# Performance work log

Hardware: AMD Instinct MI355X
Metric: run time of the kernel (lower is better)

The kernel has to match this reference:

```python
import jax, jax.numpy as jnp
import numpy as np

DIM = 384
HEADS = 12
HD = DIM // HEADS  # 32
WIN = 16
N = WIN * WIN      # 256
B = 256            # num_windows * batch
K = 5              # dwc kernel size
EPS = 1e-6


def setup_inputs() -> dict:
    key = jax.random.key(0)
    ks = jax.random.split(key, 8)
    u = lambda k, shape, fan_in: jax.random.uniform(
        k, shape, jnp.float32, -1.0 / np.sqrt(fan_in), 1.0 / np.sqrt(fan_in))
    return {
        "x": jax.random.normal(ks[0], (B, N, DIM), jnp.float32),
        # nn.Linear(dim, 3*dim): weight [3C, C], bias [3C]
        "qkv_w": u(ks[1], (3 * DIM, DIM), DIM),
        "qkv_b": u(ks[2], (3 * DIM,), DIM),
        # nn.Parameter initialized to zeros
        "pos_enc": jnp.zeros((1, N, DIM), jnp.float32),
        # depthwise Conv2d(HD, HD, K, groups=HD): weight [HD, 1, K, K]
        "dwc_w": u(ks[3], (HD, 1, K, K), K * K),
        "dwc_b": u(ks[4], (HD,), K * K),
        "proj_w": u(ks[5], (DIM, DIM), DIM),
        "proj_b": u(ks[6], (DIM,), DIM),
    }


def reference(x, qkv_w, qkv_b, pos_enc, dwc_w, dwc_b, proj_w, proj_b):
    Bsz, Nn, C = x.shape
    qkv = x @ qkv_w.T + qkv_b                     # [B, N, 3C]
    q, k, v = jnp.split(qkv, 3, axis=-1)          # each [B, N, C]
    k = k + pos_enc
    q = jax.nn.relu(q)
    k = jax.nn.relu(k)

    def to_heads(t):  # 'b n (h c) -> (b h) n c'
        return t.reshape(Bsz, Nn, HEADS, HD).transpose(0, 2, 1, 3).reshape(Bsz * HEADS, Nn, HD)

    q, k, v = to_heads(q), to_heads(k), to_heads(v)
    # explicit fp32 (autocast disabled block in original)
    qf = q.astype(jnp.float32)
    kf = k.astype(jnp.float32)
    vf = v.astype(jnp.float32)

    z = 1.0 / (jnp.einsum('bic,bc->bi', qf, kf.sum(axis=1)) + EPS)  # [BH, N]

    i = j = Nn
    c = d = HD
    if i * j * (c + d) > c * d * (i + j):  # kv-first (true for N=256, HD=32)
        kv = jnp.einsum('bjc,bjd->bcd', kf, vf)            # [BH, c, d]
        out = jnp.einsum('bic,bcd,bi->bid', qf, kv, z)     # [BH, N, d]
    else:
        qk = jnp.einsum('bic,bjc->bij', qf, kf)
        out = jnp.einsum('bij,bjd,bi->bid', qk, vf, z)

    # depthwise conv on v: 'b (w h) c -> b c w h'
    num = int(Nn ** 0.5)
    fm = vf.reshape(Bsz * HEADS, num, num, HD).transpose(0, 3, 1, 2)  # NCHW
    fm = jax.lax.conv_general_dilated(
        fm, dwc_w, window_strides=(1, 1),
        padding=[(K // 2, K // 2), (K // 2, K // 2)],
        dimension_numbers=('NCHW', 'OIHW', 'NCHW'),
        feature_group_count=HD)
    fm = fm + dwc_b[None, :, None, None]
    fm = fm.transpose(0, 2, 3, 1).reshape(Bsz * HEADS, Nn, HD)  # 'b c w h -> b (w h) c'

    out = out + fm
    # '(b h) n c -> b n (h c)'
    out = out.reshape(Bsz, HEADS, Nn, HD).transpose(0, 2, 1, 3).reshape(Bsz, Nn, C)
    return out @ proj_w.T + proj_b
```

## Files before the change

### kernel.cpp

```cpp
#include <hip/hip_runtime.h>
#include <stdint.h>
#include <stddef.h>


typedef _Float16 f16;
typedef __attribute__((ext_vector_type(4))) _Float16 f16x4;
typedef __attribute__((ext_vector_type(8))) _Float16 f16x8;
typedef __attribute__((ext_vector_type(4))) float floatx4;

#define DEV __device__ __forceinline__

DEV void async16(const void* g, void* l) {
  __builtin_amdgcn_global_load_lds(
      (const __attribute__((address_space(1))) void*)g,
      (__attribute__((address_space(3))) void*)l,
      16, 0, 0);
}

DEV floatx4 mfma16(f16x8 a, f16x8 b, floatx4 c) {
  return __builtin_amdgcn_mfma_f32_16x16x32_f16(a, b, c, 0, 0, 0);
}

DEV f16x4 cvt4(float4 v) {
  f16x4 h;
  h[0] = (f16)v.x; h[1] = (f16)v.y; h[2] = (f16)v.z; h[3] = (f16)v.w;
  return h;
}

__global__ __launch_bounds__(256) void cvt_kernel(
    const float* __restrict__ src, f16* __restrict__ dst, int n4) {
  const int stride = gridDim.x * 256;
  for (int i = blockIdx.x * 256 + threadIdx.x; i < n4; i += stride) {
    float4 v = ((const float4*)src)[i];
    ((f16x4*)dst)[i] = cvt4(v);
  }
}

__global__ __launch_bounds__(256) void qkv_kernel(
    const f16* __restrict__ A, const f16* __restrict__ W,
    const float* __restrict__ bias, const float* __restrict__ pos,
    f16* __restrict__ q_ws, f16* __restrict__ kT_ws, f16* __restrict__ vT_ws) {
  __shared__ __align__(16) f16 Af[128 * 64];
  __shared__ __align__(16) f16 Wf[128 * 64];
  const int tid = threadIdx.x;
  const int lane = tid & 63, wave = tid >> 6;
  const int quad = lane >> 4, lr = lane & 15;
  const int wm = wave >> 1, wn = wave & 1;
  const int bx = blockIdx.x;
  const int ga = bx / 72, rem = bx - ga * 72;
  const int nblk = rem >> 3, gc = rem & 7;
  const int m0 = (ga * 8 + gc) * 128, n0 = nblk * 128;
  const int rl = lane >> 3;
  const int lcol = (lane & 7) ^ rl;

  floatx4 acc[4][4] = {};

  const f16* ap[4];
  const f16* wp[4];
#pragma unroll
  for (int t2 = 0; t2 < 4; ++t2) {
    const int row = (wave * 4 + t2) * 8 + rl;
    ap[t2] = A + (size_t)(m0 + row) * 384 + lcol * 8;
    wp[t2] = W + (size_t)(n0 + row) * 384 + lcol * 8;
  }

  for (int kt = 0; kt < 6; ++kt) {
    __syncthreads();
#pragma unroll
    for (int t2 = 0; t2 < 4; ++t2) {
      const int ch = wave * 4 + t2;
      async16(ap[t2] + kt * 64, (char*)Af + ch * 1024);
      async16(wp[t2] + kt * 64, (char*)Wf + ch * 1024);
    }
    __syncthreads();
#pragma unroll
    for (int s = 0; s < 2; ++s) {
      const int pc = ((quad + s * 4) ^ (lr & 7)) * 16;
      f16x8 af[4], wf[4];
#pragma unroll
      for (int mt = 0; mt < 4; ++mt)
        af[mt] = *(const f16x8*)((const char*)Af +
                                 (wm * 64 + mt * 16 + lr) * 128 + pc);
#pragma unroll
      for (int nt = 0; nt < 4; ++nt)
        wf[nt] = *(const f16x8*)((const char*)Wf +
                                 (wn * 64 + nt * 16 + lr) * 128 + pc);
#pragma unroll
      for (int mt = 0; mt < 4; ++mt)
#pragma unroll
        for (int nt = 0; nt < 4; ++nt)
          acc[mt][nt] = mfma16(af[mt], wf[nt], acc[mt][nt]);
    }
  }

  float bv[4];
#pragma unroll
  for (int nt = 0; nt < 4; ++nt)
    bv[nt] = bias[n0 + wn * 64 + nt * 16 + lr];

  const int cls = nblk / 3;
  const int cbase = (nblk - cls * 3) * 128;
  if (cls == 0) {
#pragma unroll
    for (int mt = 0; mt < 4; ++mt) {
#pragma unroll
      for (int r = 0; r < 4; ++r) {
        const int m = m0 + wm * 64 + mt * 16 + quad * 4 + r;
        const int bwin = m >> 8, t = m & 255;
#pragma unroll
        for (int nt = 0; nt < 4; ++nt) {
          const int c = cbase + wn * 64 + nt * 16 + lr;
          const int h = c >> 5, hd = c & 31;
          const float val = fmaxf(acc[mt][nt][r] + bv[nt], 0.f);
          q_ws[(size_t)(bwin * 12 + h) * 8192 + t * 32 + hd] = (f16)val;
        }
      }
    }
  } else {
#pragma unroll
    for (int mt = 0; mt < 4; ++mt) {
      const int mb = m0 + wm * 64 + mt * 16 + quad * 4;
      const int bwin = mb >> 8, t0 = mb & 255;
#pragma unroll
      for (int nt = 0; nt < 4; ++nt) {
        const int c = cbase + wn * 64 + nt * 16 + lr;
        const int h = c >> 5, hd = c & 31;
        f16x4 pk;
        if (cls == 1) {
#pragma unroll
          for (int r = 0; r < 4; ++r)
            pk[r] = (f16)fmaxf(acc[mt][nt][r] + bv[nt] + pos[(t0 + r) * 384 + c], 0.f);
          *(f16x4*)(kT_ws + (size_t)(bwin * 12 + h) * 8192 + hd * 256 + t0) = pk;
        } else {
#pragma unroll
          for (int r = 0; r < 4; ++r)
            pk[r] = (f16)(acc[mt][nt][r] + bv[nt]);
          *(f16x4*)(vT_ws + (size_t)(bwin * 12 + h) * 8192 + hd * 256 + t0) = pk;
        }
      }
    }
  }
}

__global__ __launch_bounds__(256) void attn_kernel(
    const f16* __restrict__ q_ws, const f16* __restrict__ kT_ws,
    const f16* __restrict__ vT_ws, const float* __restrict__ dwc_w,
    const float* __restrict__ dwc_b, f16* __restrict__ y_ws) {
  __shared__ __align__(16) char khb[16640];
  __shared__ __align__(16) char vhb[16640];
  __shared__ float psum[8 * 32];
  __shared__ float ksum[4][32];
  __shared__ float zbuf[256];
  __shared__ __align__(16) f16 kvT[32 * 40];

  const int tid = threadIdx.x;
  const int lane = tid & 63, wave = tid >> 6;
  const int quad = lane >> 4, lr = lane & 15;
  const size_t base = (size_t)blockIdx.x * 8192;

#pragma unroll
  for (int t2 = 0; t2 < 4; ++t2) {
    const int is = wave * 4 + t2;
    async16(kT_ws + base + is * 512 + lane * 8, khb + is * 1040);
    async16(vT_ws + base + is * 512 + lane * 8, vhb + is * 1040);
  }
  __syncthreads();

  {
    const int c = tid & 31, seg = tid >> 5;
    const char* kr = khb + (c >> 1) * 1040 + (c & 1) * 512;
    float s = 0.f;
#pragma unroll
    for (int j8 = 0; j8 < 32; j8 += 8) {
      f16x8 a = *(const f16x8*)(kr + (seg * 32 + j8) * 2);
#pragma unroll
      for (int j = 0; j < 8; ++j) s += (float)a[j];
    }
    psum[seg * 32 + c] = s;
  }
  {
    const int m2 = wave & 1, n2 = wave >> 1;
    const int ck = m2 * 16 + lr, cv = n2 * 16 + lr;
    const char* krow = khb + (ck >> 1) * 1040 + (ck & 1) * 512;
    const char* vrow = vhb + (cv >> 1) * 1040 + (cv & 1) * 512;
    floatx4 kacc = {};
#pragma unroll
    for (int s = 0; s < 8; ++s) {
      f16x8 ka = *(const f16x8*)(krow + (s * 32 + quad * 8) * 2);
      f16x8 vb = *(const f16x8*)(vrow + (s * 32 + quad * 8) * 2);
      kacc = mfma16(ka, vb, kacc);
    }
    f16x4 kk;
#pragma unroll
    for (int r = 0; r < 4; ++r) kk[r] = (f16)kacc[r];
    *(f16x4*)(kvT + (n2 * 16 + lr) * 40 + m2 * 16 + quad * 4) = kk;
  }
  __syncthreads();

  if (lane < 32) {
    float s = 0.f;
#pragma unroll
    for (int seg = 0; seg < 8; ++seg) s += psum[seg * 32 + lane];
    ksum[wave][lane] = s;
  }

  {
    uint32_t* fmu = (uint32_t*)khb;
    const int cg = lr, xr = wave * 4 + quad, c0 = cg * 2;
    float a0[16], a1[16];
    const float b0v = dwc_b[c0], b1v = dwc_b[c0 + 1];
#pragma unroll
    for (int yy = 0; yy < 16; ++yy) { a0[yy] = b0v; a1[yy] = b1v; }
    const char* v0 = vhb + cg * 1040;
#pragma unroll
    for (int dx = 0; dx < 5; ++dx) {
      const int xx = xr + dx - 2;
      if (xx < 0 || xx > 15) continue;
      float r0[16], r1[16];
      f16x8 h0 = *(const f16x8*)(v0 + xx * 32);
      f16x8 h1 = *(const f16x8*)(v0 + xx * 32 + 16);
      f16x8 h2 = *(const f16x8*)(v0 + 512 + xx * 32);
      f16x8 h3 = *(const f16x8*)(v0 + 512 + xx * 32 + 16);
#pragma unroll
      for (int j = 0; j < 8; ++j) {
        r0[j] = (float)h0[j]; r0[8 + j] = (float)h1[j];
        r1[j] = (float)h2[j]; r1[8 + j] = (float)h3[j];
      }
#pragma unroll
      for (int dy = 0; dy < 5; ++dy) {
        const float w0 = dwc_w[c0 * 25 + dx * 5 + dy];
        const float w1 = dwc_w[(c0 + 1) * 25 + dx * 5 + dy];
#pragma unroll
        for (int yy = 0; yy < 16; ++yy) {
          const int ys = yy + dy - 2;
          if (ys >= 0 && ys < 16) {
            a0[yy] += w0 * r0[ys];
            a1[yy] += w1 * r1[ys];
          }
        }
      }
    }
#pragma unroll
    for (int yy = 0; yy < 16; ++yy) {
      const uint32_t lo = (uint32_t)__builtin_bit_cast(uint16_t, (f16)a0[yy]);
      const uint32_t hi = (uint32_t)__builtin_bit_cast(uint16_t, (f16)a1[yy]);
      fmu[(xr * 16 + yy) * 16 + cg] = lo | (hi << 16);
    }
  }

  {
    f16x8 qa[4], kb[2];
#pragma unroll
    for (int mm = 0; mm < 4; ++mm)
      qa[mm] = *(const f16x8*)(q_ws + base +
                               (size_t)(wave * 64 + mm * 16 + lr) * 32 + quad * 8);

    float ksv[8];
#pragma unroll
    for (int j = 0; j < 8; ++j) ksv[j] = ksum[wave][quad * 8 + j];
#pragma unroll
    for (int mm = 0; mm < 4; ++mm) {
      float dot = 0.f;
#pragma unroll
      for (int j = 0; j < 8; ++j) dot += (float)qa[mm][j] * ksv[j];
      dot += __shfl_xor(dot, 16);
      dot += __shfl_xor(dot, 32);
      if (quad == 0) zbuf[wave * 64 + mm * 16 + lr] = 1.f / (dot + 1e-6f);
    }

    floatx4 oacc[4][2] = {};
#pragma unroll
    for (int nt = 0; nt < 2; ++nt)
      kb[nt] = *(const f16x8*)(kvT + (nt * 16 + lr) * 40 + quad * 8);
#pragma unroll
    for (int mm = 0; mm < 4; ++mm)
#pragma unroll
      for (int nt = 0; nt < 2; ++nt)
        oacc[mm][nt] = mfma16(qa[mm], kb[nt], oacc[mm][nt]);

    const f16* fmb = (const f16*)khb;
#pragma unroll
    for (int mm = 0; mm < 4; ++mm) {
#pragma unroll
      for (int r = 0; r < 4; ++r) {
        const int i = wave * 64 + mm * 16 + quad * 4 + r;
        const float zi = zbuf[i];
#pragma unroll
        for (int nt = 0; nt < 2; ++nt) {
          const int d = nt * 16 + lr;
          const float val = oacc[mm][nt][r] * zi + (float)fmb[i * 32 + d];
          y_ws[base + (size_t)i * 32 + d] = (f16)val;
        }
      }
    }
  }
}

__global__ __launch_bounds__(256) void proj_kernel(
    const f16* __restrict__ Y, const f16* __restrict__ Wh,
    const float* __restrict__ bias, float* __restrict__ out) {
  __shared__ __align__(16) f16 Af[128 * 64];
  __shared__ __align__(16) f16 Wf[128 * 64];
  const int tid = threadIdx.x;
  const int lane = tid & 63, wave = tid >> 6;
  const int quad = lane >> 4, lr = lane & 15;
  const int wm = wave >> 1, wn = wave & 1;
  const int bx = blockIdx.x;
  const int ga = bx / 24, rem = bx - ga * 24;
  const int nblk = rem >> 3, gc = rem & 7;
  const int m0 = (ga * 8 + gc) * 128, n0 = nblk * 128;
  const int bwin = m0 >> 8, tbase = m0 & 255;
  const int rl = lane >> 3;
  const int lcol = (lane & 7) ^ rl;

  floatx4 acc[4][4] = {};

  const f16* ap[4];
  const f16* wp[4];
#pragma unroll
  for (int t2 = 0; t2 < 4; ++t2) {
    const int rowl = (wave * 4 + t2) * 8 + rl;
    ap[t2] = Y + (size_t)(bwin * 12 + (lcol >> 2)) * 8192 +
             (size_t)(tbase + rowl) * 32 + (lcol & 3) * 8;
    wp[t2] = Wh + (size_t)(n0 + rowl) * 384 + lcol * 8;
  }

  for (int kt = 0; kt < 6; ++kt) {
    __syncthreads();
#pragma unroll
    for (int t2 = 0; t2 < 4; ++t2) {
      const int ch = wave * 4 + t2;
      async16(ap[t2] + (size_t)kt * 16384, (char*)Af + ch * 1024);
      async16(wp[t2] + kt * 64, (char*)Wf + ch * 1024);
    }
    __syncthreads();
#pragma unroll
    for (int s = 0; s < 2; ++s) {
      const int pc = ((quad + s * 4) ^ (lr & 7)) * 16;
      f16x8 af[4], wf[4];
#pragma unroll
      for (int mt = 0; mt < 4; ++mt)
        af[mt] = *(const f16x8*)((const char*)Af +
                                 (wm * 64 + mt * 16 + lr) * 128 + pc);
#pragma unroll
      for (int nt = 0; nt < 4; ++nt)
        wf[nt] = *(const f16x8*)((const char*)Wf +
                                 (wn * 64 + nt * 16 + lr) * 128 + pc);
#pragma unroll
      for (int mt = 0; mt < 4; ++mt)
#pragma unroll
        for (int nt = 0; nt < 4; ++nt)
          acc[mt][nt] = mfma16(af[mt], wf[nt], acc[mt][nt]);
    }
  }

  float bv[4];
#pragma unroll
  for (int nt = 0; nt < 4; ++nt)
    bv[nt] = bias[n0 + wn * 64 + nt * 16 + lr];
#pragma unroll
  for (int mt = 0; mt < 4; ++mt)
#pragma unroll
    for (int r = 0; r < 4; ++r) {
      const int m = m0 + wm * 64 + mt * 16 + quad * 4 + r;
#pragma unroll
      for (int nt = 0; nt < 4; ++nt) {
        const int n = n0 + wn * 64 + nt * 16 + lr;
        out[(size_t)m * 384 + n] = acc[mt][nt][r] + bv[nt];
      }
    }
}

extern "C" void kernel_launch(void* const* d_in, const int* in_sizes, int n_in,
                              void* d_out, int out_size, void* d_ws, size_t ws_size,
                              hipStream_t stream) {
  const float* x = (const float*)d_in[0];
  const float* qkv_w = (const float*)d_in[1];
  const float* qkv_b = (const float*)d_in[2];
  const float* pos = (const float*)d_in[3];
  const float* dwc_w = (const float*)d_in[4];
  const float* dwc_b = (const float*)d_in[5];
  const float* proj_w = (const float*)d_in[6];
  const float* proj_b = (const float*)d_in[7];
  float* out = (float*)d_out;

  const size_t WS_NEEDED = 150994944;
  if (ws_size < WS_NEEDED) return;

  char* ws = (char*)d_ws;
  f16* q_ws = (f16*)(ws);
  f16* kT_ws = (f16*)(ws + 50331648);
  f16* vT_ws = (f16*)(ws + 100663296);

  f16* xh = (f16*)d_out;
  f16* qwh = (f16*)((char*)d_out + 50331648);
  f16* pwh = (f16*)(ws + 50331648);

  cvt_kernel<<<2048, 256, 0, stream>>>(x, xh, 6291456);
  cvt_kernel<<<432, 256, 0, stream>>>(qkv_w, qwh, 110592);
  qkv_kernel<<<4608, 256, 0, stream>>>(xh, qwh, qkv_b, pos,
                                       q_ws, kT_ws, vT_ws);
  attn_kernel<<<3072, 256, 0, stream>>>(q_ws, kT_ws, vT_ws,
                                        dwc_w, dwc_b, q_ws );
  cvt_kernel<<<144, 256, 0, stream>>>(proj_w, pwh, 36864);
  proj_kernel<<<1536, 256, 0, stream>>>(q_ws, pwh, proj_b, out);
}
```

Baseline: 351.0 us.

## Double-buffer LDS tiles in QKV and projection GEMMs to overlap loads

```diff
diff --git a/kernel.cpp b/kernel.cpp
--- a/kernel.cpp
+++ b/kernel.cpp
@@ -40,8 +40,8 @@
     const f16* __restrict__ A, const f16* __restrict__ W,
     const float* __restrict__ bias, const float* __restrict__ pos,
     f16* __restrict__ q_ws, f16* __restrict__ kT_ws, f16* __restrict__ vT_ws) {
-  __shared__ __align__(16) f16 Af[128 * 64];
-  __shared__ __align__(16) f16 Wf[128 * 64];
+  __shared__ __align__(16) f16 Af[2][128 * 64];
+  __shared__ __align__(16) f16 Wf[2][128 * 64];
   const int tid = threadIdx.x;
   const int lane = tid & 63, wave = tid >> 6;
   const int quad = lane >> 4, lr = lane & 15;
@@ -64,26 +64,36 @@
     wp[t2] = W + (size_t)(n0 + row) * 384 + lcol * 8;
   }
 
+#pragma unroll
+  for (int t2 = 0; t2 < 4; ++t2) {
+    const int ch = wave * 4 + t2;
+    async16(ap[t2], (char*)Af[0] + ch * 1024);
+    async16(wp[t2], (char*)Wf[0] + ch * 1024);
+  }
+  __syncthreads();
+
+#pragma unroll
   for (int kt = 0; kt < 6; ++kt) {
-    __syncthreads();
-#pragma unroll
-    for (int t2 = 0; t2 < 4; ++t2) {
-      const int ch = wave * 4 + t2;
-      async16(ap[t2] + kt * 64, (char*)Af + ch * 1024);
-      async16(wp[t2] + kt * 64, (char*)Wf + ch * 1024);
-    }
-    __syncthreads();
+    const int p = kt & 1;
+    if (kt < 5) {
+#pragma unroll
+      for (int t2 = 0; t2 < 4; ++t2) {
+        const int ch = wave * 4 + t2;
+        async16(ap[t2] + (kt + 1) * 64, (char*)Af[p ^ 1] + ch * 1024);
+        async16(wp[t2] + (kt + 1) * 64, (char*)Wf[p ^ 1] + ch * 1024);
+      }
+    }
 #pragma unroll
     for (int s = 0; s < 2; ++s) {
       const int pc = ((quad + s * 4) ^ (lr & 7)) * 16;
       f16x8 af[4], wf[4];
 #pragma unroll
       for (int mt = 0; mt < 4; ++mt)
-        af[mt] = *(const f16x8*)((const char*)Af +
+        af[mt] = *(const f16x8*)((const char*)Af[p] +
                                  (wm * 64 + mt * 16 + lr) * 128 + pc);
 #pragma unroll
       for (int nt = 0; nt < 4; ++nt)
-        wf[nt] = *(const f16x8*)((const char*)Wf +
+        wf[nt] = *(const f16x8*)((const char*)Wf[p] +
                                  (wn * 64 + nt * 16 + lr) * 128 + pc);
 #pragma unroll
       for (int mt = 0; mt < 4; ++mt)
@@ -91,6 +101,7 @@
         for (int nt = 0; nt < 4; ++nt)
           acc[mt][nt] = mfma16(af[mt], wf[nt], acc[mt][nt]);
     }
+    __syncthreads();
   }
 
   float bv[4];
@@ -299,8 +310,8 @@
 __global__ __launch_bounds__(256) void proj_kernel(
     const f16* __restrict__ Y, const f16* __restrict__ Wh,
     const float* __restrict__ bias, float* __restrict__ out) {
-  __shared__ __align__(16) f16 Af[128 * 64];
-  __shared__ __align__(16) f16 Wf[128 * 64];
+  __shared__ __align__(16) f16 Af[2][128 * 64];
+  __shared__ __align__(16) f16 Wf[2][128 * 64];
   const int tid = threadIdx.x;
   const int lane = tid & 63, wave = tid >> 6;
   const int quad = lane >> 4, lr = lane & 15;
@@ -325,26 +336,36 @@
     wp[t2] = Wh + (size_t)(n0 + rowl) * 384 + lcol * 8;
   }
 
+#pragma unroll
+  for (int t2 = 0; t2 < 4; ++t2) {
+    const int ch = wave * 4 + t2;
+    async16(ap[t2], (char*)Af[0] + ch * 1024);
+    async16(wp[t2], (char*)Wf[0] + ch * 1024);
+  }
+  __syncthreads();
+
+#pragma unroll
   for (int kt = 0; kt < 6; ++kt) {
-    __syncthreads();
-#pragma unroll
-    for (int t2 = 0; t2 < 4; ++t2) {
-      const int ch = wave * 4 + t2;
-      async16(ap[t2] + (size_t)kt * 16384, (char*)Af + ch * 1024);
-      async16(wp[t2] + kt * 64, (char*)Wf + ch * 1024);
-    }
-    __syncthreads();
+    const int p = kt & 1;
+    if (kt < 5) {
+#pragma unroll
+      for (int t2 = 0; t2 < 4; ++t2) {
+        const int ch = wave * 4 + t2;
+        async16(ap[t2] + (size_t)(kt + 1) * 16384, (char*)Af[p ^ 1] + ch * 1024);
+        async16(wp[t2] + (kt + 1) * 64, (char*)Wf[p ^ 1] + ch * 1024);
+      }
+    }
 #pragma unroll
     for (int s = 0; s < 2; ++s) {
       const int pc = ((quad + s * 4) ^ (lr & 7)) * 16;
       f16x8 af[4], wf[4];
 #pragma unroll
       for (int mt = 0; mt < 4; ++mt)
-        af[mt] = *(const f16x8*)((const char*)Af +
+        af[mt] = *(const f16x8*)((const char*)Af[p] +
                                  (wm * 64 + mt * 16 + lr) * 128 + pc);
 #pragma unroll
       for (int nt = 0; nt < 4; ++nt)
-        wf[nt] = *(const f16x8*)((const char*)Wf +
+        wf[nt] = *(const f16x8*)((const char*)Wf[p] +
                                  (wn * 64 + nt * 16 + lr) * 128 + pc);
 #pragma unroll
       for (int mt = 0; mt < 4; ++mt)
@@ -352,6 +373,7 @@
         for (int nt = 0; nt < 4; ++nt)
           acc[mt][nt] = mfma16(af[mt], wf[nt], acc[mt][nt]);
     }
+    __syncthreads();
   }
 
   float bv[4];
```

After: 359.7 us. 2.5% more time.
